# Kernel tuning notes

Hardware: AMD Instinct MI355X
Metric: run time of the kernel (lower is better)

The kernel has to match this reference:

```python
import jax, jax.numpy as jnp
import numpy as np

B, NA, NB, E = 2, 256, 256, 512
H1, H2 = 300, 100


def setup_inputs() -> dict:
    key = jax.random.key(0)
    ks = jax.random.split(key, 16)

    def n(k, shape, scale=1.0):
        return jax.random.normal(k, shape, dtype=jnp.float32) * scale

    z = lambda shape: jnp.zeros(shape, jnp.float32)
    return {
        "action_embedding": n(ks[0], (B, E, NA)),
        "anchor_embedding": n(ks[1], (B, E, NB)),
        "action_points": n(ks[2], (B, 3, NA)),
        "anchor_points": n(ks[3], (B, 3, NB)),
        # pairwise MLP kernel params: 2E -> 300 -> 100 -> 1
        "mlp_W1": n(ks[4], (2 * E, H1), (2 * E) ** -0.5),
        "mlp_b1": z((H1,)),
        "mlp_W2": n(ks[5], (H1, H2), H1 ** -0.5),
        "mlp_b2": z((H2,)),
        "mlp_W3": n(ks[6], (H2, 1), H2 ** -0.5),
        "mlp_b3": z((1,)),
        # PointNet [512,64,64,64,128,512] (1x1 convs) + Conv1d(512,1,bias=False)
        "pn_W0": n(ks[7], (64, 512), 512 ** -0.5),
        "pn_b0": z((64,)),
        "pn_W1": n(ks[8], (64, 64), 64 ** -0.5),
        "pn_b1": z((64,)),
        "pn_W2": n(ks[9], (64, 64), 64 ** -0.5),
        "pn_b2": z((64,)),
        "pn_W3": n(ks[10], (128, 64), 64 ** -0.5),
        "pn_b3": z((128,)),
        "pn_W4": n(ks[11], (512, 128), 128 ** -0.5),
        "pn_b4": z((512,)),
        "head_W": n(ks[12], (1, 512), 512 ** -0.5),
    }


def reference(action_embedding, anchor_embedding, action_points, anchor_points,
              mlp_W1, mlp_b1, mlp_W2, mlp_b2, mlp_W3, mlp_b3,
              pn_W0, pn_b0, pn_W1, pn_b1, pn_W2, pn_b2, pn_W3, pn_b3,
              pn_W4, pn_b4, head_W):
    P_A = action_points.transpose(0, 2, 1)      # (B, NA, 3)
    P_B = anchor_points.transpose(0, 2, 1)      # (B, NB, 3)
    Phi_A = action_embedding.transpose(0, 2, 1)  # (B, NA, E)
    Phi_B = anchor_embedding.transpose(0, 2, 1)  # (B, NB, E)
    Ed = Phi_A.shape[-1]

    # --- symmetric pairwise MLP kernel: softplus((mlp(cat(a,b)) + mlp(cat(b,a))) / 2) ---
    # First Linear layer is split so the O(NA*NB*2E) concat is never materialized:
    # cat(a,b) @ W1 == a @ W1[:E] + b @ W1[E:]
    W1a, W1b = mlp_W1[:Ed], mlp_W1[Ed:]

    def mlp_tail(h):  # h: (B, NA, NB, H1) pre-activation of layer 1
        h = jax.nn.relu(h)
        h = jax.nn.relu(h @ mlp_W2 + mlp_b2)
        return (h @ mlp_W3 + mlp_b3)[..., 0]  # (B, NA, NB)

    hA_a = Phi_A @ W1a  # (B, NA, H1)
    hA_b = Phi_A @ W1b
    hB_a = Phi_B @ W1a  # (B, NB, H1)
    hB_b = Phi_B @ W1b
    v1 = mlp_tail(hA_a[:, :, None, :] + hB_b[:, None, :, :] + mlp_b1)  # mlp(cat(x1,x2))
    v2 = mlp_tail(hB_a[:, None, :, :] + hA_b[:, :, None, :] + mlp_b1)  # mlp(cat(x2,x1))
    R_est = jax.nn.softplus((v1 + v2) * 0.5)  # (B, NA, NB) estimated distances

    # --- weighted multilateration (estimate_p), vectorized over (B, NA) ---
    # Linearized LS: ||p||^2 - 2 q_k^T p = r_k^2 - ||q_k||^2; subtract weighted means
    # to eliminate ||p||^2, then solve 3x3 weighted normal equations per action point.
    w = jnp.ones(P_B.shape[:2], R_est.dtype)            # (B, NB) uniform weights (last_attn=False)
    wsum = w.sum(-1, keepdims=True)                      # (B, 1)
    qbar = (w[..., None] * P_B).sum(1) / wsum            # (B, 3)
    bvec = (P_B ** 2).sum(-1)[:, None, :] - R_est ** 2   # (B, NA, NB)
    bbar = (w[:, None, :] * bvec).sum(-1) / wsum         # (B, NA)
    Amat = 2.0 * (P_B - qbar[:, None, :])                # (B, NB, 3)
    yvec = bvec - bbar[..., None]                        # (B, NA, NB)
    M = jnp.einsum('bki,bk,bkj->bij', Amat, w, Amat)     # (B, 3, 3)
    rhs = jnp.einsum('bki,bk,bak->bai', Amat, w, yvec)   # (B, NA, 3)
    P_A_B_pred = jnp.linalg.solve(M[:, None], rhs[..., None])[..., 0]  # (B, NA, 3)

    flow = (P_A_B_pred - P_A).transpose(0, 2, 1)         # (B, 3, NA)

    # --- PointNet flow-weight head (1x1 convs + ReLU, final conv no bias) ---
    x = action_embedding                                  # (B, 512, NA)
    for Wc, bc in ((pn_W0, pn_b0), (pn_W1, pn_b1), (pn_W2, pn_b2),
                   (pn_W3, pn_b3), (pn_W4, pn_b4)):
        x = jax.nn.relu(jnp.einsum('oi,bin->bon', Wc, x) + bc[None, :, None])
    weight = jnp.einsum('oi,bin->bon', head_W, x)        # (B, 1, NA)

    full_flow = jnp.concatenate([flow, weight], axis=1)  # (B, 4, NA)
    return full_flow
```

## Files before the change

### kernel.cpp

```cpp
#include <hip/hip_runtime.h>
#include <hip/hip_bf16.h>
#include <hip/hip_fp16.h>

typedef float f32x4 __attribute__((ext_vector_type(4)));
typedef float f32x16 __attribute__((ext_vector_type(16)));
typedef short s16x8 __attribute__((ext_vector_type(8)));
typedef _Float16 f16x8 __attribute__((ext_vector_type(8)));

#define OFF_EMBT   0u
#define OFF_W1T    1048576u
#define OFF_W2TSW  1662976u
#define OFF_W0BF   1740800u
#define OFF_HA     1806336u
#define OFF_R2     3051520u
#define WS_TOTAL   3575808u

__device__ __forceinline__ int pack_bf2(float a, float b) {
  __hip_bfloat162 h = __float22bfloat162_rn(make_float2(a, b));
  int r; __builtin_memcpy(&r, &h, 4); return r;
}
__device__ __forceinline__ unsigned pack_f16_2(float a, float b) {
  __half2 h = __float22half2_rn(make_float2(a, b));
  unsigned r; __builtin_memcpy(&r, &h, 4); return r;
}
__device__ __forceinline__ unsigned short bf16u(float f) {
  __hip_bfloat16 h = __float2bfloat16(f);
  unsigned short u; __builtin_memcpy(&u, &h, 2); return u;
}
__device__ __forceinline__ s16x8 i4_to_s8(int a, int b, int c, int d) {
  union { int i[4]; s16x8 s; } u;
  u.i[0] = a; u.i[1] = b; u.i[2] = c; u.i[3] = d; return u.s;
}
template<int CTRL>
__device__ __forceinline__ float dpp_add(float x) {
  int xi; __builtin_memcpy(&xi, &x, 4);
  int yi = __builtin_amdgcn_update_dpp(0, xi, CTRL, 0xf, 0xf, true);
  float y; __builtin_memcpy(&y, &yi, 4);
  return x + y;
}
__device__ __forceinline__ float swz_xor16(float x) {
  int xi; __builtin_memcpy(&xi, &x, 4);
  int yi = __builtin_amdgcn_ds_swizzle(xi, 0x401f);
  float y; __builtin_memcpy(&y, &yi, 4);
  return y;
}

__global__ __launch_bounds__(256) void ka_prep(
    const float* __restrict__ act_emb, const float* __restrict__ anc_emb,
    const float* __restrict__ W1, const float* __restrict__ W2,
    const float* __restrict__ W0pn, char* __restrict__ ws)
{
  __hip_bfloat16* embT  = (__hip_bfloat16*)(ws + OFF_EMBT);
  __hip_bfloat16* W1T   = (__hip_bfloat16*)(ws + OFF_W1T);
  unsigned short* W2Tsw = (unsigned short*)(ws + OFF_W2TSW);
  unsigned short* W0bf  = (unsigned short*)(ws + OFF_W0BF);
  __shared__ float tile[64][65];
  int blk = blockIdx.x, t = threadIdx.x;
  if (blk < 128) {
    int b = blk >> 6, emb = (blk >> 5) & 1, ntile = (blk >> 3) & 3, etile = blk & 7;
    const float* src = emb ? anc_emb : act_emb;
    int e0 = etile * 64, n0 = ntile * 64;
    int rr = t >> 6, cc = t & 63;
    #pragma unroll
    for (int it2 = 0; it2 < 16; ++it2) {
      int e_l = rr * 16 + it2;
      tile[e_l][cc] = src[(size_t)(b * 512 + e0 + e_l) * 256 + n0 + cc];
    }
    __syncthreads();
    int n_l = t >> 2, eq = t & 3;
    unsigned int* dst = (unsigned int*)(embT + ((size_t)((b * 2 + emb) * 256 + n0 + n_l)) * 512 + e0 + eq * 16);
    #pragma unroll
    for (int kk = 0; kk < 8; ++kk)
      dst[kk] = (unsigned)pack_bf2(tile[eq * 16 + 2 * kk][n_l], tile[eq * 16 + 2 * kk + 1][n_l]);
  } else if (blk < 208) {
    int id = blk - 128;
    int half = id / 40; int rem = id % 40; int et = rem / 5; int ct = rem % 5;
    int e0 = et * 64, c0 = ct * 64;
    int rr = t >> 6, cc = t & 63;
    #pragma unroll
    for (int it2 = 0; it2 < 16; ++it2) {
      int e_l = rr * 16 + it2;
      int c = c0 + cc;
      tile[e_l][cc] = (c < 300) ? W1[(size_t)(half * 512 + e0 + e_l) * 300 + c] : 0.f;
    }
    __syncthreads();
    int c_l = t >> 2, eq = t & 3;
    if (c0 + c_l < 300) {
      unsigned int* dst = (unsigned int*)(W1T + ((size_t)(half * 300 + c0 + c_l)) * 512 + e0 + eq * 16);
      #pragma unroll
      for (int kk = 0; kk < 8; ++kk)
        dst[kk] = (unsigned)pack_bf2(tile[eq * 16 + 2 * kk][c_l], tile[eq * 16 + 2 * kk + 1][c_l]);
    }
  } else if (blk < 227) {
    int idx = (blk - 208) * 256 + t;
    int lane = idx & 63; int ntks = idx >> 6; int nt = ntks & 3; int ks = ntks >> 2;
    int n = nt * 32 + (lane & 31);
    int kb = ks * 16 + (lane >> 5) * 8;
    unsigned int q[4];
    #pragma unroll
    for (int jj = 0; jj < 4; ++jj) {
      int k0 = kb + jj * 2, k1 = kb + jj * 2 + 1;
      float f0 = (n < 100 && k0 < 300) ? W2[(size_t)k0 * 100 + n] : 0.f;
      float f1 = (n < 100 && k1 < 300) ? W2[(size_t)k1 * 100 + n] : 0.f;
      q[jj] = pack_f16_2(f0, f1);
    }
    ((uint4*)W2Tsw)[idx] = make_uint4(q[0], q[1], q[2], q[3]);
  } else if (blk < 243) {
    int idx = (blk - 227) * 256 + t;
    const float* s = W0pn + (size_t)idx * 8;
    ((uint4*)W0bf)[idx] = make_uint4(
        (unsigned)pack_bf2(s[0], s[1]), (unsigned)pack_bf2(s[2], s[3]),
        (unsigned)pack_bf2(s[4], s[5]), (unsigned)pack_bf2(s[6], s[7]));
  } else {
    int idx = (blk - 243) * 256 + t;
    _Float16* haf = (_Float16*)(ws + OFF_HA);
    #pragma unroll
    for (int u2 = 0; u2 < 2; ++u2) {
      int unit = idx * 2 + u2;
      int combo = unit >> 5, row = unit & 31;
      size_t off = (((size_t)combo * 19 + 18) << 9) + (1 << 8) + (row << 3) + 4;
      unsigned* p = (unsigned*)(haf + off);
      p[0] = 0u; p[1] = 0u;
    }
  }
}

template<int K, int NT>
__device__ __forceinline__ void pn_layer(unsigned short* xb, const float* __restrict__ W,
                                         const float* __restrict__ bias, int wv, int l, int g)
{
  constexpr int NN = NT / 4;
  f32x4 z = {0.f, 0.f, 0.f, 0.f};
  f32x4 acc[NN];
  #pragma unroll
  for (int nn = 0; nn < NN; ++nn) acc[nn] = z;
  #pragma unroll
  for (int nn = 0; nn < NN; ++nn) {
    int o = (wv + nn * 4) * 16 + l;
    const float* wr0 = W + (size_t)o * K;
    #pragma unroll
    for (int ks = 0; ks < K / 32; ++ks) {
      int koff = ks * 32 + g * 8;
      f32x4 wa = *(const f32x4*)(wr0 + koff);
      f32x4 wb = *(const f32x4*)(wr0 + koff + 4);
      s16x8 bfr = i4_to_s8(pack_bf2(wa.x, wa.y), pack_bf2(wa.z, wa.w),
                           pack_bf2(wb.x, wb.y), pack_bf2(wb.z, wb.w));
      s16x8 a0 = *(const s16x8*)(xb + (size_t)l * 520 + koff);
      acc[nn] = __builtin_amdgcn_mfma_f32_16x16x32_bf16(a0, bfr, acc[nn], 0, 0, 0);
    }
  }
  __syncthreads();
  #pragma unroll
  for (int nn = 0; nn < NN; ++nn) {
    int chan = (wv + nn * 4) * 16 + l;
    float bv = bias[chan];
    #pragma unroll
    for (int r = 0; r < 4; ++r)
      xb[(size_t)(g * 4 + r) * 520 + chan] = bf16u(fmaxf(acc[nn][r] + bv, 0.f));
  }
  __syncthreads();
}

__global__ __launch_bounds__(256) void k1_ha(
    const __hip_bfloat16* __restrict__ embT, const __hip_bfloat16* __restrict__ W1T,
    const float* __restrict__ b1, _Float16* __restrict__ ha_f,
    const unsigned short* __restrict__ W0bf,
    const float* __restrict__ pnW1, const float* __restrict__ pnW2,
    const float* __restrict__ pnW3, const float* __restrict__ pnW4,
    const float* __restrict__ pnB0, const float* __restrict__ pnB1,
    const float* __restrict__ pnB2, const float* __restrict__ pnB3,
    const float* __restrict__ pnB4,
    const float* __restrict__ headW, float* __restrict__ out)
{
  __shared__ unsigned short xbuf[16 * 520];
  int blk = blockIdx.x, t = threadIdx.x;
  int wv = t >> 6, lane = t & 63, l = lane & 15, g = lane >> 4;
  if (blk < 320) {
    int b = blk / 160; int r = blk % 160; int emb = r / 80; r %= 80;
    int mch = r / 5; int nch = r % 5;
    int m0 = mch * 16;
    const unsigned short* Ap = (const unsigned short*)embT +
        ((size_t)((b * 2 + emb) * 256 + m0 + l)) * 512;
    const unsigned short* Wp = (const unsigned short*)W1T;
    f32x4 z = {0.f, 0.f, 0.f, 0.f};
    f32x4 acc[2] = {z, z};
    for (int ks = 0; ks < 16; ++ks) {
      int k0 = ks * 32 + g * 8;
      s16x8 af = *(const s16x8*)(Ap + k0);
      #pragma unroll
      for (int q = 0; q < 2; ++q) {
        int c = nch * 120 + (wv * 2 + q) * 16 + l;
        s16x8 bf = {0, 0, 0, 0, 0, 0, 0, 0};
        if (c < 600) bf = *(const s16x8*)(Wp + (size_t)c * 512 + k0);
        acc[q] = __builtin_amdgcn_mfma_f32_16x16x32_bf16(af, bf, acc[q], 0, 0, 0);
      }
    }
    #pragma unroll
    for (int q = 0; q < 2; ++q) {
      int cl = (wv * 2 + q) * 16 + l;
      int c = nch * 120 + cl;
      if (cl < 120 && c < 600) {
        int half = (c >= 300) ? 1 : 0;
        int cc = c - half * 300;
        float bias = (emb == 0) ? b1[cc] : 0.f;
        int d = emb * 2 + half;
        int ksf = cc >> 4, hi2 = (cc >> 3) & 1, e = cc & 7;
        #pragma unroll
        for (int r2 = 0; r2 < 4; ++r2) {
          int i = m0 + g * 4 + r2;
          size_t off = (((((size_t)(b * 4 + d)) * 8 + (i >> 5)) * 19 + ksf) << 9)
                     + (hi2 << 8) + ((i & 31) << 3) + e;
          ha_f[off] = (_Float16)__float2half_rn(acc[q][r2] + bias);
        }
      }
    }
  } else {
    int pn = blk - 320;
    int b_pn = pn >> 4, n0 = (pn & 15) * 16;
    unsigned short* xb = xbuf;
    {
      const unsigned short* A0 = (const unsigned short*)embT + ((size_t)(b_pn * 2 * 256 + n0)) * 512;
      f32x4 acc0 = {0.f, 0.f, 0.f, 0.f};
      int o = wv * 16 + l;
      const unsigned short* w0r = W0bf + (size_t)o * 512;
      #pragma unroll
      for (int ks = 0; ks < 16; ++ks) {
        int koff = ks * 32 + g * 8;
        s16x8 bfr = *(const s16x8*)(w0r + koff);
        s16x8 a0 = *(const s16x8*)(A0 + (size_t)l * 512 + koff);
        acc0 = __builtin_amdgcn_mfma_f32_16x16x32_bf16(a0, bfr, acc0, 0, 0, 0);
      }
      float bv = pnB0[o];
      #pragma unroll
      for (int r2 = 0; r2 < 4; ++r2)
        xb[(size_t)(g * 4 + r2) * 520 + o] = bf16u(fmaxf(acc0[r2] + bv, 0.f));
      __syncthreads();
    }
    pn_layer<64, 4>(xb, pnW1, pnB1, wv, l, g);
    pn_layer<64, 4>(xb, pnW2, pnB2, wv, l, g);
    pn_layer<64, 8>(xb, pnW3, pnB3, wv, l, g);
    pn_layer<128, 32>(xb, pnW4, pnB4, wv, l, g);
    {
      int p_l = t >> 4, os = t & 15;
      const unsigned short* row = xb + (size_t)p_l * 520 + os * 32;
      float s = 0.f;
      #pragma unroll
      for (int c = 0; c < 32; ++c) {
        unsigned int u = ((unsigned int)row[c]) << 16;
        float xv; __builtin_memcpy(&xv, &u, 4);
        s += xv * headW[os * 32 + c];
      }
      s += __shfl_xor(s, 1); s += __shfl_xor(s, 2);
      s += __shfl_xor(s, 4); s += __shfl_xor(s, 8);
      if (os == 0) out[(size_t)(b_pn * 4 + 3) * 256 + n0 + p_l] = s;
    }
  }
}

__global__ __launch_bounds__(512, 4) void k2_main(
    const _Float16* __restrict__ haF, const unsigned short* __restrict__ W2Tsw,
    const float* __restrict__ b2g, const float* __restrict__ W3g, const float* __restrict__ b3g,
    float* __restrict__ R2)
{
  __shared__ int4 w2s[4864];
  __shared__ float ex[4][2][16];
  int blkp = blockIdx.x, t = threadIdx.x;
  int blk = (blkp & 7) * 64 + (blkp >> 3);
  int wv = t >> 6, lane = t & 63, col = lane & 31, hi = lane >> 5;
  int jl = wv & 3, dir = wv >> 2;
  int u = blk; int b = u >> 8; u &= 255; int it = u >> 5; int jtp = u & 31;
  int i0 = it * 32;
  int j0 = jtp * 8 + jl;
  {
    const int4* w2g = (const int4*)W2Tsw;
    #pragma unroll
    for (int q = 0; q < 9; ++q) { int idx = t + q * 512; w2s[idx] = w2g[idx]; }
    { int idx = t + 9 * 512; if (idx < 4864) w2s[idx] = w2g[idx]; }
  }
  const _Float16* pA = haF + ((((size_t)(b * 4 + dir)) * 8 + it) * 19) * 512 + lane * 8;
  const _Float16* pB0 = haF + ((((size_t)(b * 4 + (3 - dir))) * 8 + (j0 >> 5)) * 19) * 512
                        + (hi * 32 + (j0 & 31)) * 8;
  __syncthreads();

  const f16x8 zf = {0, 0, 0, 0, 0, 0, 0, 0};
  f32x16 z16;
  #pragma unroll
  for (int q = 0; q < 16; ++q) z16[q] = 0.f;
  float b3 = b3g[0];

  #pragma unroll 1
  for (int s = 0; s < 2; ++s) {
    const _Float16* pBs = pB0 + s * 32;
    f16x8 aC = *(const f16x8*)(pA);
    f16x8 aN = *(const f16x8*)(pA + 512);
    f16x8 bC = *(const f16x8*)(pBs);
    f16x8 bN = *(const f16x8*)(pBs + 512);
    f32x16 acc0 = z16, acc1 = z16, acc2 = z16, acc3 = z16;
    #pragma unroll 2
    for (int ks = 0; ks < 19; ++ks) {
      f16x8 aN2, bN2;
      if (ks <= 16) {
        aN2 = *(const f16x8*)(pA + (ks + 2) * 512);
        bN2 = *(const f16x8*)(pBs + (ks + 2) * 512);
      } else { aN2 = aC; bN2 = bC; }
      f16x8 af = __builtin_elementwise_max(aC + bC, zf);
      const int4* wp = &w2s[ks * 256 + lane];
      f16x8 bf0 = *(const f16x8*)(wp);
      f16x8 bf1 = *(const f16x8*)(wp + 64);
      f16x8 bf2 = *(const f16x8*)(wp + 128);
      f16x8 bf3 = *(const f16x8*)(wp + 192);
      acc0 = __builtin_amdgcn_mfma_f32_32x32x16_f16(af, bf0, acc0, 0, 0, 0);
      acc1 = __builtin_amdgcn_mfma_f32_32x32x16_f16(af, bf1, acc1, 0, 0, 0);
      acc2 = __builtin_amdgcn_mfma_f32_32x32x16_f16(af, bf2, acc2, 0, 0, 0);
      acc3 = __builtin_amdgcn_mfma_f32_32x32x16_f16(af, bf3, acc3, 0, 0, 0);
      aC = aN; aN = aN2; bC = bN; bN = bN2;
    }
    int j = j0 + s * 4;
    float w3v[4], b2v[4];
    #pragma unroll
    for (int nt = 0; nt < 4; ++nt) {
      int n = nt * 32 + col;
      w3v[nt] = (n < 100) ? W3g[n] : 0.f;
      b2v[nt] = (n < 100) ? b2g[n] : 0.f;
    }
    float mine = 0.f;
    #pragma unroll
    for (int r = 0; r < 16; ++r) {
      float x = fmaxf(acc0[r] + b2v[0], 0.f) * w3v[0]
              + fmaxf(acc1[r] + b2v[1], 0.f) * w3v[1]
              + fmaxf(acc2[r] + b2v[2], 0.f) * w3v[2]
              + fmaxf(acc3[r] + b2v[3], 0.f) * w3v[3];
      x = dpp_add<0xB1>(x);
      x = dpp_add<0x4E>(x);
      x = dpp_add<0x141>(x);
      x = dpp_add<0x140>(x);
      x += swz_xor16(x);
      if (col == r) mine = x;
    }
    __syncthreads();
    if (dir == 1 && col < 16) ex[jl][hi][col] = mine;
    __syncthreads();
    if (dir == 0 && col < 16) {
      float tot = mine + ex[jl][hi][col];
      float S = 0.5f * tot + b3;
      float Rr = (S > 20.f) ? S : log1pf(expf(S));
      int il = (col & 3) + 8 * (col >> 2) + 4 * hi;
      R2[((size_t)(b * 256 + i0 + il)) * 256 + j] = Rr * Rr;
    }
  }
}

__device__ __forceinline__ float block_sum(float v, float* redbuf, int t) {
  #pragma unroll
  for (int m = 1; m < 64; m <<= 1) v += __shfl_xor(v, m);
  __syncthreads();
  if ((t & 63) == 0) redbuf[t >> 6] = v;
  __syncthreads();
  return redbuf[0] + redbuf[1] + redbuf[2] + redbuf[3];
}

__global__ __launch_bounds__(256) void k3_solve(
    const float* __restrict__ anc_pts, const float* __restrict__ act_pts,
    const float* __restrict__ R2, float* __restrict__ out)
{
  __shared__ float Ax[256], Ay[256], Az[256];
  __shared__ float redbuf[4];
  int blk = blockIdx.x, t = threadIdx.x;
  int b = blk >> 2, ic = blk & 3;
  int k = t;
  float px = anc_pts[(size_t)(b * 3 + 0) * 256 + k];
  float py = anc_pts[(size_t)(b * 3 + 1) * 256 + k];
  float pz = anc_pts[(size_t)(b * 3 + 2) * 256 + k];
  float qx = block_sum(px, redbuf, t) * (1.f / 256.f);
  float qy = block_sum(py, redbuf, t) * (1.f / 256.f);
  float qz = block_sum(pz, redbuf, t) * (1.f / 256.f);
  float ax = 2.f * (px - qx), ay = 2.f * (py - qy), az = 2.f * (pz - qz);
  float p2 = px * px + py * py + pz * pz;
  Ax[k] = ax; Ay[k] = ay; Az[k] = az;
  float mxx = block_sum(ax * ax, redbuf, t);
  float mxy = block_sum(ax * ay, redbuf, t);
  float mxz = block_sum(ax * az, redbuf, t);
  float myy = block_sum(ay * ay, redbuf, t);
  float myz = block_sum(ay * az, redbuf, t);
  float mzz = block_sum(az * az, redbuf, t);
  float c0x = block_sum(ax * p2, redbuf, t);
  float c0y = block_sum(ay * p2, redbuf, t);
  float c0z = block_sum(az * p2, redbuf, t);
  __syncthreads();
  float det = mxx * (myy * mzz - myz * myz) - mxy * (mxy * mzz - myz * mxz) + mxz * (mxy * myz - myy * mxz);
  float idet = 1.f / det;
  float i00 = (myy * mzz - myz * myz) * idet;
  float i01 = (mxz * myz - mxy * mzz) * idet;
  float i02 = (mxy * myz - mxz * myy) * idet;
  float i11 = (mxx * mzz - mxz * mxz) * idet;
  float i12 = (mxy * mxz - mxx * myz) * idet;
  float i22 = (mxx * myy - mxy * mxy) * idet;
  int il = t >> 2, ks = t & 3;
  int i = ic * 64 + il;
  const float* rrow = R2 + ((size_t)(b * 256 + i)) * 256;
  float r0 = 0.f, r1 = 0.f, r2 = 0.f;
  #pragma unroll
  for (int kk = 0; kk < 16; ++kk) {
    int kb = ks * 64 + kk * 4;
    f32x4 rv = *(const f32x4*)(rrow + kb);
    r0 += Ax[kb] * rv.x + Ax[kb + 1] * rv.y + Ax[kb + 2] * rv.z + Ax[kb + 3] * rv.w;
    r1 += Ay[kb] * rv.x + Ay[kb + 1] * rv.y + Ay[kb + 2] * rv.z + Ay[kb + 3] * rv.w;
    r2 += Az[kb] * rv.x + Az[kb + 1] * rv.y + Az[kb + 2] * rv.z + Az[kb + 3] * rv.w;
  }
  r0 += __shfl_xor(r0, 1); r0 += __shfl_xor(r0, 2);
  r1 += __shfl_xor(r1, 1); r1 += __shfl_xor(r1, 2);
  r2 += __shfl_xor(r2, 1); r2 += __shfl_xor(r2, 2);
  if (ks == 0) {
    float hx = c0x - r0, hy = c0y - r1, hz = c0z - r2;
    float x0 = i00 * hx + i01 * hy + i02 * hz;
    float x1 = i01 * hx + i11 * hy + i12 * hz;
    float x2 = i02 * hx + i12 * hy + i22 * hz;
    out[(size_t)(b * 4 + 0) * 256 + i] = x0 - act_pts[(size_t)(b * 3 + 0) * 256 + i];
    out[(size_t)(b * 4 + 1) * 256 + i] = x1 - act_pts[(size_t)(b * 3 + 1) * 256 + i];
    out[(size_t)(b * 4 + 2) * 256 + i] = x2 - act_pts[(size_t)(b * 3 + 2) * 256 + i];
  }
}

extern "C" void kernel_launch(void* const* d_in, const int* in_sizes, int n_in,
                              void* d_out, int out_size, void* d_ws, size_t ws_size,
                              hipStream_t stream)
{
  const float* act_emb = (const float*)d_in[0];
  const float* anc_emb = (const float*)d_in[1];
  const float* act_pts = (const float*)d_in[2];
  const float* anc_pts = (const float*)d_in[3];
  const float* W1  = (const float*)d_in[4];
  const float* b1  = (const float*)d_in[5];
  const float* W2  = (const float*)d_in[6];
  const float* b2  = (const float*)d_in[7];
  const float* W3  = (const float*)d_in[8];
  const float* b3  = (const float*)d_in[9];
  const float* pnW0 = (const float*)d_in[10];
  const float* pnB0 = (const float*)d_in[11];
  const float* pnW1 = (const float*)d_in[12];
  const float* pnB1 = (const float*)d_in[13];
  const float* pnW2 = (const float*)d_in[14];
  const float* pnB2 = (const float*)d_in[15];
  const float* pnW3 = (const float*)d_in[16];
  const float* pnB3 = (const float*)d_in[17];
  const float* pnW4 = (const float*)d_in[18];
  const float* pnB4 = (const float*)d_in[19];
  const float* headW = (const float*)d_in[20];
  char* ws = (char*)d_ws;
  __hip_bfloat16* embT  = (__hip_bfloat16*)(ws + OFF_EMBT);
  __hip_bfloat16* W1T   = (__hip_bfloat16*)(ws + OFF_W1T);
  unsigned short* W2Tsw = (unsigned short*)(ws + OFF_W2TSW);
  unsigned short* W0bf  = (unsigned short*)(ws + OFF_W0BF);
  _Float16* ha_f = (_Float16*)(ws + OFF_HA);
  float* R2ws  = (float*)(ws + OFF_R2);
  float* outp  = (float*)d_out;

  ka_prep<<<247, 256, 0, stream>>>(act_emb, anc_emb, W1, W2, pnW0, ws);
  k1_ha<<<352, 256, 0, stream>>>(embT, W1T, b1, ha_f, W0bf,
                                 pnW1, pnW2, pnW3, pnW4, pnB0, pnB1, pnB2, pnB3, pnB4,
                                 headW, outp);
  k2_main<<<512, 512, 0, stream>>>(ha_f, W2Tsw, b2, W3, b3, R2ws);
  k3_solve<<<8, 256, 0, stream>>>(anc_pts, act_pts, R2ws, outp);
}
```

Before: 170.8 us.

## Compute both MLP directions per wave, dropping LDS exchange and pair loop

Each wave now computes both symmetric directions (a,b) and (b,a) for a single j column in one K loop, using eight accumulators instead of four. Previously, waves were split by direction, each looped over two j values, and the halves were combined through shared memory with two block barriers. The change removes that LDS exchange and the barriers, and reuses each W2 fragment read from LDS for two MFMAs. In exchange, register pressure doubles and the occupancy hint drops from 4 to 2 blocks per SM, and prefetch depth falls from two stages to one.

```diff
diff --git a/kernel.cpp b/kernel.cpp
--- a/kernel.cpp
+++ b/kernel.cpp
@@ -257,65 +257,71 @@
   }
 }
 
-__global__ __launch_bounds__(512, 4) void k2_main(
+__global__ __launch_bounds__(512, 2) void k2_main(
     const _Float16* __restrict__ haF, const unsigned short* __restrict__ W2Tsw,
     const float* __restrict__ b2g, const float* __restrict__ W3g, const float* __restrict__ b3g,
     float* __restrict__ R2)
 {
   __shared__ int4 w2s[4864];
-  __shared__ float ex[4][2][16];
   int blkp = blockIdx.x, t = threadIdx.x;
   int blk = (blkp & 7) * 64 + (blkp >> 3);
   int wv = t >> 6, lane = t & 63, col = lane & 31, hi = lane >> 5;
-  int jl = wv & 3, dir = wv >> 2;
   int u = blk; int b = u >> 8; u &= 255; int it = u >> 5; int jtp = u & 31;
   int i0 = it * 32;
-  int j0 = jtp * 8 + jl;
+  int j = jtp * 8 + wv;
   {
     const int4* w2g = (const int4*)W2Tsw;
     #pragma unroll
     for (int q = 0; q < 9; ++q) { int idx = t + q * 512; w2s[idx] = w2g[idx]; }
     { int idx = t + 9 * 512; if (idx < 4864) w2s[idx] = w2g[idx]; }
   }
-  const _Float16* pA = haF + ((((size_t)(b * 4 + dir)) * 8 + it) * 19) * 512 + lane * 8;
-  const _Float16* pB0 = haF + ((((size_t)(b * 4 + (3 - dir))) * 8 + (j0 >> 5)) * 19) * 512
-                        + (hi * 32 + (j0 & 31)) * 8;
+  const _Float16* pA0 = haF + ((((size_t)(b * 4 + 0)) * 8 + it) * 19) * 512 + lane * 8;
+  const _Float16* pA1 = haF + ((((size_t)(b * 4 + 1)) * 8 + it) * 19) * 512 + lane * 8;
+  const _Float16* pB0 = haF + ((((size_t)(b * 4 + 3)) * 8 + (j >> 5)) * 19) * 512
+                        + (hi * 32 + (j & 31)) * 8;
+  const _Float16* pB1 = haF + ((((size_t)(b * 4 + 2)) * 8 + (j >> 5)) * 19) * 512
+                        + (hi * 32 + (j & 31)) * 8;
+  f16x8 a0c = *(const f16x8*)(pA0);
+  f16x8 a1c = *(const f16x8*)(pA1);
+  f16x8 b0c = *(const f16x8*)(pB0);
+  f16x8 b1c = *(const f16x8*)(pB1);
   __syncthreads();
 
   const f16x8 zf = {0, 0, 0, 0, 0, 0, 0, 0};
   f32x16 z16;
   #pragma unroll
   for (int q = 0; q < 16; ++q) z16[q] = 0.f;
-  float b3 = b3g[0];
+  f32x16 acc00 = z16, acc01 = z16, acc02 = z16, acc03 = z16;
+  f32x16 acc10 = z16, acc11 = z16, acc12 = z16, acc13 = z16;
 
   #pragma unroll 1
-  for (int s = 0; s < 2; ++s) {
-    const _Float16* pBs = pB0 + s * 32;
-    f16x8 aC = *(const f16x8*)(pA);
-    f16x8 aN = *(const f16x8*)(pA + 512);
-    f16x8 bC = *(const f16x8*)(pBs);
-    f16x8 bN = *(const f16x8*)(pBs + 512);
-    f32x16 acc0 = z16, acc1 = z16, acc2 = z16, acc3 = z16;
-    #pragma unroll 2
-    for (int ks = 0; ks < 19; ++ks) {
-      f16x8 aN2, bN2;
-      if (ks <= 16) {
-        aN2 = *(const f16x8*)(pA + (ks + 2) * 512);
-        bN2 = *(const f16x8*)(pBs + (ks + 2) * 512);
-      } else { aN2 = aC; bN2 = bC; }
-      f16x8 af = __builtin_elementwise_max(aC + bC, zf);
-      const int4* wp = &w2s[ks * 256 + lane];
-      f16x8 bf0 = *(const f16x8*)(wp);
-      f16x8 bf1 = *(const f16x8*)(wp + 64);
-      f16x8 bf2 = *(const f16x8*)(wp + 128);
-      f16x8 bf3 = *(const f16x8*)(wp + 192);
-      acc0 = __builtin_amdgcn_mfma_f32_32x32x16_f16(af, bf0, acc0, 0, 0, 0);
-      acc1 = __builtin_amdgcn_mfma_f32_32x32x16_f16(af, bf1, acc1, 0, 0, 0);
-      acc2 = __builtin_amdgcn_mfma_f32_32x32x16_f16(af, bf2, acc2, 0, 0, 0);
-      acc3 = __builtin_amdgcn_mfma_f32_32x32x16_f16(af, bf3, acc3, 0, 0, 0);
-      aC = aN; aN = aN2; bC = bN; bN = bN2;
-    }
-    int j = j0 + s * 4;
+  for (int ks = 0; ks < 19; ++ks) {
+    f16x8 a0n, a1n, b0n, b1n;
+    if (ks < 18) {
+      int ko = (ks + 1) * 512;
+      a0n = *(const f16x8*)(pA0 + ko);
+      a1n = *(const f16x8*)(pA1 + ko);
+      b0n = *(const f16x8*)(pB0 + ko);
+      b1n = *(const f16x8*)(pB1 + ko);
+    } else { a0n = a0c; a1n = a1c; b0n = b0c; b1n = b1c; }
+    f16x8 af0 = __builtin_elementwise_max(a0c + b0c, zf);
+    f16x8 af1 = __builtin_elementwise_max(a1c + b1c, zf);
+    const int4* wp = &w2s[ks * 256 + lane];
+    f16x8 bf0 = *(const f16x8*)(wp);
+    f16x8 bf1 = *(const f16x8*)(wp + 64);
+    f16x8 bf2 = *(const f16x8*)(wp + 128);
+    f16x8 bf3 = *(const f16x8*)(wp + 192);
+    acc00 = __builtin_amdgcn_mfma_f32_32x32x16_f16(af0, bf0, acc00, 0, 0, 0);
+    acc10 = __builtin_amdgcn_mfma_f32_32x32x16_f16(af1, bf0, acc10, 0, 0, 0);
+    acc01 = __builtin_amdgcn_mfma_f32_32x32x16_f16(af0, bf1, acc01, 0, 0, 0);
+    acc11 = __builtin_amdgcn_mfma_f32_32x32x16_f16(af1, bf1, acc11, 0, 0, 0);
+    acc02 = __builtin_amdgcn_mfma_f32_32x32x16_f16(af0, bf2, acc02, 0, 0, 0);
+    acc12 = __builtin_amdgcn_mfma_f32_32x32x16_f16(af1, bf2, acc12, 0, 0, 0);
+    acc03 = __builtin_amdgcn_mfma_f32_32x32x16_f16(af0, bf3, acc03, 0, 0, 0);
+    acc13 = __builtin_amdgcn_mfma_f32_32x32x16_f16(af1, bf3, acc13, 0, 0, 0);
+    a0c = a0n; a1c = a1n; b0c = b0n; b1c = b1n;
+  }
+  {
     float w3v[4], b2v[4];
     #pragma unroll
     for (int nt = 0; nt < 4; ++nt) {
@@ -323,13 +329,14 @@
       w3v[nt] = (n < 100) ? W3g[n] : 0.f;
       b2v[nt] = (n < 100) ? b2g[n] : 0.f;
     }
+    float b3 = b3g[0];
     float mine = 0.f;
     #pragma unroll
     for (int r = 0; r < 16; ++r) {
-      float x = fmaxf(acc0[r] + b2v[0], 0.f) * w3v[0]
-              + fmaxf(acc1[r] + b2v[1], 0.f) * w3v[1]
-              + fmaxf(acc2[r] + b2v[2], 0.f) * w3v[2]
-              + fmaxf(acc3[r] + b2v[3], 0.f) * w3v[3];
+      float x = fmaxf(acc00[r] + b2v[0], 0.f) * w3v[0] + fmaxf(acc10[r] + b2v[0], 0.f) * w3v[0]
+              + fmaxf(acc01[r] + b2v[1], 0.f) * w3v[1] + fmaxf(acc11[r] + b2v[1], 0.f) * w3v[1]
+              + fmaxf(acc02[r] + b2v[2], 0.f) * w3v[2] + fmaxf(acc12[r] + b2v[2], 0.f) * w3v[2]
+              + fmaxf(acc03[r] + b2v[3], 0.f) * w3v[3] + fmaxf(acc13[r] + b2v[3], 0.f) * w3v[3];
       x = dpp_add<0xB1>(x);
       x = dpp_add<0x4E>(x);
       x = dpp_add<0x141>(x);
@@ -337,12 +344,8 @@
       x += swz_xor16(x);
       if (col == r) mine = x;
     }
-    __syncthreads();
-    if (dir == 1 && col < 16) ex[jl][hi][col] = mine;
-    __syncthreads();
-    if (dir == 0 && col < 16) {
-      float tot = mine + ex[jl][hi][col];
-      float S = 0.5f * tot + b3;
+    if (col < 16) {
+      float S = 0.5f * mine + b3;
       float Rr = (S > 20.f) ? S : log1pf(expf(S));
       int il = (col & 3) + 8 * (col >> 2) + 4 * hi;
       R2[((size_t)(b * 256 + i0 + il)) * 256 + j] = Rr * Rr;
```

New measurement: 155.2 us. 9.2% less time.
